# Optimization experiments

Measured on AMD Instinct MI355X. Metric: run time of the kernel, lower is better.

Reference implementation:

```python
import jax, jax.numpy as jnp
import numpy as np

B, T = 4096, 256
COND, INTV, H = 128, 64, 256


def _glorot(key, shape):
    fan_in = shape[0]
    return jax.random.normal(key, shape, dtype=jnp.float32) / np.sqrt(fan_in)


def setup_inputs() -> dict:
    key = jax.random.key(0)
    ks = jax.random.split(key, 20)
    inp = {
        "cond": jax.random.normal(ks[0], (B, COND), dtype=jnp.float32),
        "interval_feat": jax.random.normal(ks[1], (B, INTV), dtype=jnp.float32),
        "times": jnp.cumsum(jax.random.uniform(ks[2], (B, T), dtype=jnp.float32), axis=1),
        "seq_lens": jax.random.randint(ks[3], (B,), 1, T + 1),
        # seq_feature MLP: INTV -> 2*INTV -> 2*INTV -> INTV
        "w1": _glorot(ks[4], (INTV, 2 * INTV)), "b1": jnp.zeros((2 * INTV,), jnp.float32),
        "w2": _glorot(ks[5], (2 * INTV, 2 * INTV)), "b2": jnp.zeros((2 * INTV,), jnp.float32),
        "w3": _glorot(ks[6], (2 * INTV, INTV)), "b3": jnp.zeros((INTV,), jnp.float32),
        # h0 projection: (COND+INTV) -> H
        "w_h0": _glorot(ks[7], (COND + INTV, H)), "b_h0": jnp.zeros((H,), jnp.float32),
        # GRUCell (input dim 1), gate order r,z,n
        "w_ih": _glorot(ks[8], (1, 3 * H)), "b_ih": jnp.zeros((3 * H,), jnp.float32),
        "w_hh": _glorot(ks[9], (H, 3 * H)), "b_hh": jnp.zeros((3 * H,), jnp.float32),
        # head: H -> 2 (delta, stop logit)
        "w_head": _glorot(ks[10], (H, 2)), "b_head": jnp.zeros((2,), jnp.float32),
    }
    return inp


def reference(cond, interval_feat, times, seq_lens,
              w1, b1, w2, b2, w3, b3, w_h0, b_h0,
              w_ih, w_hh, b_ih, b_hh, w_head, b_head):
    # seq_feature MLP
    s = jax.nn.relu(interval_feat @ w1 + b1)
    s = jax.nn.relu(s @ w2 + b2)
    seq_emb = s @ w3 + b3
    # initial hidden state
    h0 = jnp.tanh(jnp.concatenate([cond, seq_emb], axis=-1) @ w_h0 + b_h0)  # (B,H)
    # ground-truth deltas; step 0 input is 0, step i>=1 input is gt_delta[:, i-1]
    gt_delta = jnp.diff(times, axis=1, prepend=jnp.zeros((times.shape[0], 1), times.dtype))  # (B,T)
    xs = jnp.concatenate([jnp.zeros((1, times.shape[0]), times.dtype), gt_delta.T], axis=0)  # (T+1,B)

    def step(h, x):
        gi = x[:, None] * w_ih[0] + b_ih          # (B,3H)
        gh = h @ w_hh + b_hh                       # (B,3H)
        gi_r, gi_z, gi_n = jnp.split(gi, 3, axis=-1)
        gh_r, gh_z, gh_n = jnp.split(gh, 3, axis=-1)
        r = jax.nn.sigmoid(gi_r + gh_r)
        z = jax.nn.sigmoid(gi_z + gh_z)
        n = jnp.tanh(gi_n + r * gh_n)
        h_new = (1.0 - z) * n + z * h
        out = h_new @ w_head + b_head              # (B,2)
        return h_new, out

    _, outs = jax.lax.scan(step, h0, xs)           # outs: (T+1,B,2)
    pred_delta = outs[:, :, 0].T                   # (B,T+1)
    stop_logits = outs[:, :, 1].T                  # (B,T+1)
    return pred_delta, stop_logits
```

## Files before the change

kernel.cpp:

```cpp
#include <hip/hip_runtime.h>
#include <cstddef>

typedef _Float16 f16x8 __attribute__((ext_vector_type(8)));
typedef float    f32x4 __attribute__((ext_vector_type(4)));

#define Bc 4096
#define Tc 256
#define NSTEP 257
#define RB 16
#define HSTR 264
#define HEAD_OFF 393216

__device__ inline float sigm(float x)  { return __builtin_amdgcn_rcpf(1.f + __expf(-x)); }
__device__ inline float tanh_(float x) { return 1.f - 2.f * __builtin_amdgcn_rcpf(1.f + __expf(2.f * x)); }

__global__ __launch_bounds__(256) void build_frags(
    const float* __restrict__ w_hh, const float* __restrict__ w_head,
    _Float16* __restrict__ ws)
{
    int flat = blockIdx.x * 256 + threadIdx.x;
    if (blockIdx.x < 96) {
        int f    = flat >> 6;
        int lane = flat & 63;
        int kt   = f & 7;
        int nc   = (f >> 3) % 3;
        int trio = f / 24;
        int c     = nc * 256 + trio * 16 + (lane & 15);
        int kbase = kt * 32 + (lane >> 4) * 8;
        _Float16* dst = ws + (size_t)f * 512 + (size_t)lane * 8;
        #pragma unroll
        for (int j = 0; j < 8; ++j)
            dst[j] = (_Float16)w_hh[(size_t)(kbase + j) * 768 + c];
    } else {
        int idx = flat - 96 * 256;
        int kt   = idx >> 6;
        int lane = idx & 63;
        int col   = lane & 15;
        int kbase = kt * 32 + (lane >> 4) * 8;
        _Float16* dst = ws + HEAD_OFF / 2 + (size_t)kt * 512 + (size_t)lane * 8;
        #pragma unroll
        for (int j = 0; j < 8; ++j)
            dst[j] = (col < 2) ? (_Float16)w_head[(size_t)(kbase + j) * 2 + col]
                               : (_Float16)0.f;
    }
}

__global__ __attribute__((amdgpu_waves_per_eu(2, 2))) __launch_bounds__(512)
void gru_mfma(
    const float* __restrict__ cond, const float* __restrict__ ivf,
    const float* __restrict__ times,
    const float* __restrict__ w1, const float* __restrict__ b1,
    const float* __restrict__ w2, const float* __restrict__ b2,
    const float* __restrict__ w3, const float* __restrict__ b3,
    const float* __restrict__ wh0, const float* __restrict__ bh0,
    const float* __restrict__ w_ih, const float* __restrict__ b_ih,
    const float* __restrict__ b_hh, const float* __restrict__ b_head,
    const _Float16* __restrict__ wfrag,
    float* __restrict__ out)
{
    __shared__ __align__(16) _Float16 hA[RB * HSTR];
    __shared__ __align__(16) _Float16 hB[RB * HSTR];
    __shared__ float  xs[RB * NSTEP];
    __shared__ __align__(16) _Float16 headB[4096];
    __shared__ float  gateC[256 * 8];
    __shared__ float  outbuf[2][RB][16];
    __shared__ float  bh2[2];
    __shared__ float  mlp1[RB * 128];
    __shared__ float  mlp2[RB * 128];
    __shared__ float  embS[RB * 64];
    __shared__ float  h0f[RB * 256];

    const int tid  = threadIdx.x;
    const int w    = tid >> 6;
    const int lane = tid & 63;
    const int l15  = lane & 15;
    const int q    = lane >> 4;
    const int row0 = blockIdx.x * RB;

    for (int o = tid; o < RB * 128; o += 512) {
        int r = o >> 7, c = o & 127;
        float a = b1[c];
        #pragma unroll 4
        for (int k = 0; k < 64; ++k)
            a = fmaf(ivf[(size_t)(row0 + r) * 64 + k], w1[k * 128 + c], a);
        mlp1[o] = fmaxf(a, 0.f);
    }
    __syncthreads();
    for (int o = tid; o < RB * 128; o += 512) {
        int r = o >> 7, c = o & 127;
        float a = b2[c];
        #pragma unroll 4
        for (int k = 0; k < 128; ++k)
            a = fmaf(mlp1[r * 128 + k], w2[k * 128 + c], a);
        mlp2[o] = fmaxf(a, 0.f);
    }
    __syncthreads();
    for (int o = tid; o < RB * 64; o += 512) {
        int r = o >> 6, c = o & 63;
        float a = b3[c];
        #pragma unroll 4
        for (int k = 0; k < 128; ++k)
            a = fmaf(mlp2[r * 128 + k], w3[k * 64 + c], a);
        embS[o] = a;
    }
    __syncthreads();
    for (int o = tid; o < RB * 256; o += 512) {
        int r = o >> 8, c = o & 255;
        float a = bh0[c];
        #pragma unroll 4
        for (int k = 0; k < 128; ++k)
            a = fmaf(cond[(size_t)(row0 + r) * 128 + k], wh0[k * 256 + c], a);
        #pragma unroll 4
        for (int k = 0; k < 64; ++k)
            a = fmaf(embS[r * 64 + k], wh0[(128 + k) * 256 + c], a);
        h0f[o] = tanh_(a);
    }
    __syncthreads();

    for (int o = tid; o < RB * 256; o += 512) {
        int r = o >> 8, c = o & 255;
        hA[r * HSTR + c] = (_Float16)h0f[o];
    }
    for (int o = tid; o < RB * NSTEP; o += 512) {
        int r = o / NSTEP, ii = o - r * NSTEP;
        float x = 0.f;
        if (ii >= 1) {
            float a = times[(size_t)(row0 + r) * Tc + (ii - 1)];
            float b = (ii >= 2) ? times[(size_t)(row0 + r) * Tc + (ii - 2)] : 0.f;
            x = a - b;
        }
        xs[o] = x;
    }
    {
        const float4* src = (const float4*)(wfrag + HEAD_OFF / 2);
        ((float4*)headB)[tid] = src[tid];
    }
    for (int uu = tid; uu < 256; uu += 512) {
        gateC[uu * 8 + 0] = w_ih[uu];
        gateC[uu * 8 + 1] = w_ih[256 + uu];
        gateC[uu * 8 + 2] = w_ih[512 + uu];
        gateC[uu * 8 + 3] = b_ih[uu] + b_hh[uu];
        gateC[uu * 8 + 4] = b_ih[256 + uu] + b_hh[256 + uu];
        gateC[uu * 8 + 5] = b_ih[512 + uu];
        gateC[uu * 8 + 6] = b_hh[512 + uu];
        gateC[uu * 8 + 7] = 0.f;
    }
    if (tid < 2) bh2[tid] = b_head[tid];

    const int u0 = w * 32 + l15;
    const int u1 = u0 + 16;

    f16x8 Bf[2][3][8];
    #pragma unroll
    for (int p = 0; p < 2; ++p)
        #pragma unroll
        for (int nc = 0; nc < 3; ++nc)
            #pragma unroll
            for (int kt = 0; kt < 8; ++kt)
                Bf[p][nc][kt] = *(const f16x8*)(wfrag
                    + (size_t)(((2 * w + p) * 3 + nc) * 8 + kt) * 512
                    + (size_t)lane * 8);

    __syncthreads();

    float hold[2][4];
    #pragma unroll
    for (int p = 0; p < 2; ++p)
        #pragma unroll
        for (int j = 0; j < 4; ++j)
            hold[p][j] = h0f[(q * 4 + j) * 256 + (p ? u1 : u0)];

    auto STEP = [&](const _Float16* hc, _Float16* hn, int i) {
        const bool doGh = (i < NSTEP);
        const bool doHd = (i >= 1) && (w == 0);

        f32x4 aR[2], aZ[2], aN[2];
        #pragma unroll
        for (int p = 0; p < 2; ++p) {
            aR[p] = (f32x4){0.f, 0.f, 0.f, 0.f};
            aZ[p] = (f32x4){0.f, 0.f, 0.f, 0.f};
            aN[p] = (f32x4){0.f, 0.f, 0.f, 0.f};
        }
        f32x4 aH = (f32x4){0.f, 0.f, 0.f, 0.f};

        __builtin_amdgcn_s_setprio(1);
        #pragma unroll
        for (int kt = 0; kt < 8; ++kt) {
            if (doGh || doHd) {
                f16x8 Af = *(const f16x8*)(hc + l15 * HSTR + kt * 32 + q * 8);
                if (doGh) {
                    #pragma unroll
                    for (int p = 0; p < 2; ++p) {
                        aR[p] = __builtin_amdgcn_mfma_f32_16x16x32_f16(Af, Bf[p][0][kt], aR[p], 0, 0, 0);
                        aZ[p] = __builtin_amdgcn_mfma_f32_16x16x32_f16(Af, Bf[p][1][kt], aZ[p], 0, 0, 0);
                        aN[p] = __builtin_amdgcn_mfma_f32_16x16x32_f16(Af, Bf[p][2][kt], aN[p], 0, 0, 0);
                    }
                }
                if (doHd) {
                    f16x8 Bh = *(const f16x8*)(headB + kt * 512 + lane * 8);
                    aH = __builtin_amdgcn_mfma_f32_16x16x32_f16(Af, Bh, aH, 0, 0, 0);
                }
            }
        }
        __builtin_amdgcn_s_setprio(0);

        if (doHd) {
            const int o = i - 1;
            if (l15 < 2) {
                #pragma unroll
                for (int j = 0; j < 4; ++j)
                    outbuf[l15][q * 4 + j][o & 15] = aH[j];
            }
            if (((o & 15) == 15) || (o == NSTEP - 1)) {
                const int cnt   = (o & 15) + 1;
                const int obase = o & ~15;
                #pragma unroll
                for (int s = 0; s < 8; ++s) {
                    const int idx   = s * 64 + lane;
                    const int e     = idx & 15;
                    const int row   = (idx >> 4) & 15;
                    const int plane = idx >> 8;
                    if (e < cnt)
                        out[(size_t)plane * ((size_t)Bc * NSTEP)
                            + (size_t)(row0 + row) * NSTEP + obase + e]
                            = outbuf[plane][row][e] + bh2[plane];
                }
            }
        }

        if (doGh) {
            #pragma unroll
            for (int p = 0; p < 2; ++p) {
                const int u = p ? u1 : u0;
                const f32x4 g0 = *(const f32x4*)(gateC + u * 8);
                const f32x4 g1 = *(const f32x4*)(gateC + u * 8 + 4);
                #pragma unroll
                for (int j = 0; j < 4; ++j) {
                    const int m = q * 4 + j;
                    const float x  = xs[m * NSTEP + i];
                    const float rr = sigm(fmaf(x, g0[0], g0[3]) + aR[p][j]);
                    const float zz = sigm(fmaf(x, g0[1], g1[0]) + aZ[p][j]);
                    const float nn = tanh_(fmaf(x, g0[2], g1[1]) + rr * (aN[p][j] + g1[2]));
                    const float hn_ = nn + zz * (hold[p][j] - nn);
                    hold[p][j] = hn_;
                    hn[m * HSTR + u] = (_Float16)hn_;
                }
            }
        }
        __syncthreads();
    };

    for (int i = 0; i < NSTEP + 1; i += 2) {
        STEP(hA, hB, i);
        STEP(hB, hA, i + 1);
    }
}

extern "C" void kernel_launch(void* const* d_in, const int* in_sizes, int n_in,
                              void* d_out, int out_size, void* d_ws, size_t ws_size,
                              hipStream_t stream) {
    const float* cond   = (const float*)d_in[0];
    const float* ivf    = (const float*)d_in[1];
    const float* times  = (const float*)d_in[2];
    const float* w1     = (const float*)d_in[4];
    const float* b1     = (const float*)d_in[5];
    const float* w2     = (const float*)d_in[6];
    const float* b2     = (const float*)d_in[7];
    const float* w3     = (const float*)d_in[8];
    const float* b3     = (const float*)d_in[9];
    const float* wh0    = (const float*)d_in[10];
    const float* bh0    = (const float*)d_in[11];
    const float* w_ih   = (const float*)d_in[12];
    const float* b_ih   = (const float*)d_in[13];
    const float* w_hh   = (const float*)d_in[14];
    const float* b_hh   = (const float*)d_in[15];
    const float* w_head = (const float*)d_in[16];
    const float* b_head = (const float*)d_in[17];

    float*    outp = (float*)d_out;
    _Float16* ws   = (_Float16*)d_ws;

    build_frags<<<98, 256, 0, stream>>>(w_hh, w_head, ws);
    gru_mfma<<<Bc / RB, 512, 0, stream>>>(cond, ivf, times,
                                          w1, b1, w2, b2, w3, b3, wh0, bh0,
                                          w_ih, b_ih, b_hh, b_head,
                                          (const _Float16*)ws, outp);
}
```

Measured before the change: 849.8 us.

## Spread head output flush across all waves and prefetch A fragments in GRU step

Head outputs now go into a double-buffered outbuf, and every 16 steps all 512 threads write the previous 16-step tile to global memory. Before, wave 0 alone wrote it inside the step, which put it on the critical path. The A-fragment LDS loads are software-pipelined one k-tile ahead, and the setprio calls are removed. The per-step input deltas are repacked so each lane reads its four rows with a single float4 load. The flush timing across steps and the final-column write add indexing complexity that must stay consistent with the step loop.

```diff
diff --git a/kernel.cpp b/kernel.cpp
--- a/kernel.cpp
+++ b/kernel.cpp
@@ -60,10 +60,10 @@
 {
     __shared__ __align__(16) _Float16 hA[RB * HSTR];
     __shared__ __align__(16) _Float16 hB[RB * HSTR];
-    __shared__ float  xs[RB * NSTEP];
+    __shared__ __align__(16) float xs4[4 * NSTEP * 4];
     __shared__ __align__(16) _Float16 headB[4096];
     __shared__ float  gateC[256 * 8];
-    __shared__ float  outbuf[2][RB][16];
+    __shared__ float  outbuf[2][2][RB][16];
     __shared__ float  bh2[2];
     __shared__ float  mlp1[RB * 128];
     __shared__ float  mlp2[RB * 128];
@@ -121,15 +121,19 @@
         int r = o >> 8, c = o & 255;
         hA[r * HSTR + c] = (_Float16)h0f[o];
     }
-    for (int o = tid; o < RB * NSTEP; o += 512) {
-        int r = o / NSTEP, ii = o - r * NSTEP;
-        float x = 0.f;
-        if (ii >= 1) {
-            float a = times[(size_t)(row0 + r) * Tc + (ii - 1)];
-            float b = (ii >= 2) ? times[(size_t)(row0 + r) * Tc + (ii - 2)] : 0.f;
-            x = a - b;
-        }
-        xs[o] = x;
+    for (int o = tid; o < 4 * NSTEP; o += 512) {
+        int qg = o / NSTEP, ii = o - qg * NSTEP;
+        #pragma unroll
+        for (int jj = 0; jj < 4; ++jj) {
+            int r = qg * 4 + jj;
+            float x = 0.f;
+            if (ii >= 1) {
+                float a = times[(size_t)(row0 + r) * Tc + (ii - 1)];
+                float b = (ii >= 2) ? times[(size_t)(row0 + r) * Tc + (ii - 2)] : 0.f;
+                x = a - b;
+            }
+            xs4[o * 4 + jj] = x;
+        }
     }
     {
         const float4* src = (const float4*)(wfrag + HEAD_OFF / 2);
@@ -171,6 +175,17 @@
             hold[p][j] = h0f[(q * 4 + j) * 256 + (p ? u1 : u0)];
 
     auto STEP = [&](const _Float16* hc, _Float16* hn, int i) {
+        if (i >= 2 && ((i - 2) & 15) == 15) {
+            const int obase = i - 17;
+            const int par   = (obase >> 4) & 1;
+            const int e     = tid & 15;
+            const int row   = (tid >> 4) & 15;
+            const int plane = tid >> 8;
+            out[(size_t)plane * ((size_t)Bc * NSTEP)
+                + (size_t)(row0 + row) * NSTEP + obase + e]
+                = outbuf[par][plane][row][e] + bh2[plane];
+        }
+
         const bool doGh = (i < NSTEP);
         const bool doHd = (i >= 1) && (w == 0);
 
@@ -183,52 +198,36 @@
         }
         f32x4 aH = (f32x4){0.f, 0.f, 0.f, 0.f};
 
-        __builtin_amdgcn_s_setprio(1);
+        const _Float16* abase = hc + l15 * HSTR + q * 8;
+        f16x8 Afc = *(const f16x8*)(abase);
         #pragma unroll
         for (int kt = 0; kt < 8; ++kt) {
-            if (doGh || doHd) {
-                f16x8 Af = *(const f16x8*)(hc + l15 * HSTR + kt * 32 + q * 8);
-                if (doGh) {
-                    #pragma unroll
-                    for (int p = 0; p < 2; ++p) {
-                        aR[p] = __builtin_amdgcn_mfma_f32_16x16x32_f16(Af, Bf[p][0][kt], aR[p], 0, 0, 0);
-                        aZ[p] = __builtin_amdgcn_mfma_f32_16x16x32_f16(Af, Bf[p][1][kt], aZ[p], 0, 0, 0);
-                        aN[p] = __builtin_amdgcn_mfma_f32_16x16x32_f16(Af, Bf[p][2][kt], aN[p], 0, 0, 0);
-                    }
+            f16x8 Afn;
+            if (kt < 7) Afn = *(const f16x8*)(abase + (kt + 1) * 32);
+            if (doGh) {
+                #pragma unroll
+                for (int p = 0; p < 2; ++p) {
+                    aR[p] = __builtin_amdgcn_mfma_f32_16x16x32_f16(Afc, Bf[p][0][kt], aR[p], 0, 0, 0);
+                    aZ[p] = __builtin_amdgcn_mfma_f32_16x16x32_f16(Afc, Bf[p][1][kt], aZ[p], 0, 0, 0);
+                    aN[p] = __builtin_amdgcn_mfma_f32_16x16x32_f16(Afc, Bf[p][2][kt], aN[p], 0, 0, 0);
                 }
-                if (doHd) {
-                    f16x8 Bh = *(const f16x8*)(headB + kt * 512 + lane * 8);
-                    aH = __builtin_amdgcn_mfma_f32_16x16x32_f16(Af, Bh, aH, 0, 0, 0);
-                }
-            }
-        }
-        __builtin_amdgcn_s_setprio(0);
-
-        if (doHd) {
+            }
+            if (doHd) {
+                f16x8 Bh = *(const f16x8*)(headB + kt * 512 + lane * 8);
+                aH = __builtin_amdgcn_mfma_f32_16x16x32_f16(Afc, Bh, aH, 0, 0, 0);
+            }
+            Afc = Afn;
+        }
+
+        if (doHd && l15 < 2) {
             const int o = i - 1;
-            if (l15 < 2) {
-                #pragma unroll
-                for (int j = 0; j < 4; ++j)
-                    outbuf[l15][q * 4 + j][o & 15] = aH[j];
-            }
-            if (((o & 15) == 15) || (o == NSTEP - 1)) {
-                const int cnt   = (o & 15) + 1;
-                const int obase = o & ~15;
-                #pragma unroll
-                for (int s = 0; s < 8; ++s) {
-                    const int idx   = s * 64 + lane;
-                    const int e     = idx & 15;
-                    const int row   = (idx >> 4) & 15;
-                    const int plane = idx >> 8;
-                    if (e < cnt)
-                        out[(size_t)plane * ((size_t)Bc * NSTEP)
-                            + (size_t)(row0 + row) * NSTEP + obase + e]
-                            = outbuf[plane][row][e] + bh2[plane];
-                }
-            }
+            #pragma unroll
+            for (int j = 0; j < 4; ++j)
+                outbuf[(o >> 4) & 1][l15][q * 4 + j][o & 15] = aH[j];
         }
 
         if (doGh) {
+            const f32x4 xv = *(const f32x4*)(xs4 + (q * NSTEP + i) * 4);
             #pragma unroll
             for (int p = 0; p < 2; ++p) {
                 const int u = p ? u1 : u0;
@@ -237,7 +236,7 @@
                 #pragma unroll
                 for (int j = 0; j < 4; ++j) {
                     const int m = q * 4 + j;
-                    const float x  = xs[m * NSTEP + i];
+                    const float x  = xv[j];
                     const float rr = sigm(fmaf(x, g0[0], g0[3]) + aR[p][j]);
                     const float zz = sigm(fmaf(x, g0[1], g1[0]) + aZ[p][j]);
                     const float nn = tanh_(fmaf(x, g0[2], g1[1]) + rr * (aN[p][j] + g1[2]));
@@ -253,6 +252,17 @@
     for (int i = 0; i < NSTEP + 1; i += 2) {
         STEP(hA, hB, i);
         STEP(hB, hA, i + 1);
+    }
+
+    {
+        const int e     = tid & 15;
+        const int row   = (tid >> 4) & 15;
+        const int plane = tid >> 8;
+        if (e < 1) {
+            out[(size_t)plane * ((size_t)Bc * NSTEP)
+                + (size_t)(row0 + row) * NSTEP + 256 + e]
+                = outbuf[0][plane][row][e] + bh2[plane];
+        }
     }
 }
 
```

New measurement: 836.2 us. No clear change (-1.6%).
